# Kernel tuning notes

Measured on AMD Instinct MI355X. Metric: run time of the kernel, lower is better.

Reference implementation:

```python
import jax, jax.numpy as jnp
import numpy as np

SPATIAL_SHAPES = [(100, 152), (50, 76), (25, 38), (13, 19)]
D_MODEL = 256
N_HEADS = 8
N_LEVELS = 4
N_POINTS = 4
D_FFN = 1024
D_HEAD = D_MODEL // N_HEADS
EPS = 1e-5


def layernorm(x, g, b):
    mu = jnp.mean(x, axis=-1, keepdims=True)
    var = jnp.var(x, axis=-1, keepdims=True)
    return (x - mu) * jax.lax.rsqrt(var + EPS) * g + b


def bilinear_sample(value_l, H, W, locs):
    # value_l: (N, H*W, nH, dH); locs: (N, Lq, nH, P, 2) normalized to [0,1]
    # Matches torch grid_sample(align_corners=False, padding_mode='zeros') with grid=2*loc-1.
    N, Lq = locs.shape[0], locs.shape[1]
    x = locs[..., 0] * W - 0.5  # (N, Lq, nH, P) pixel coords
    y = locs[..., 1] * H - 0.5
    x0 = jnp.floor(x)
    y0 = jnp.floor(y)
    fx = x - x0
    fy = y - y0
    x0 = x0.astype(jnp.int32)
    y0 = y0.astype(jnp.int32)
    out = jnp.zeros((N, Lq, N_POINTS, N_HEADS, D_HEAD), value_l.dtype)
    for dy in (0, 1):
        for dx in (0, 1):
            xi = x0 + dx
            yi = y0 + dy
            w = (fx if dx else 1.0 - fx) * (fy if dy else 1.0 - fy)
            valid = (xi >= 0) & (xi < W) & (yi >= 0) & (yi < H)
            idx = jnp.clip(yi, 0, H - 1) * W + jnp.clip(xi, 0, W - 1)  # (N, Lq, nH, P)
            idx = idx.transpose(0, 1, 3, 2).reshape(N, Lq * N_POINTS, N_HEADS, 1)
            g = jnp.take_along_axis(value_l, idx, axis=1)  # (N, Lq*P, nH, dH)
            g = g.reshape(N, Lq, N_POINTS, N_HEADS, D_HEAD)
            wv = jnp.where(valid, w, 0.0).transpose(0, 1, 3, 2)[..., None]  # (N, Lq, P, nH, 1)
            out = out + g * wv
    return out  # (N, Lq, P, nH, dH)


def msdeform_attn(query, value_in, ref_points,
                  w_value, b_value, w_off, b_off, w_attn, b_attn, w_out, b_out):
    N, Lq, _ = query.shape
    value = (value_in @ w_value + b_value).reshape(N, -1, N_HEADS, D_HEAD)
    off = (query @ w_off + b_off).reshape(N, Lq, N_HEADS, N_LEVELS, N_POINTS, 2)
    attn = (query @ w_attn + b_attn).reshape(N, Lq, N_HEADS, N_LEVELS * N_POINTS)
    attn = jax.nn.softmax(attn, axis=-1).reshape(N, Lq, N_HEADS, N_LEVELS, N_POINTS)
    # offset normalizer is (W, H) per level
    norm = jnp.array([[w, h] for (h, w) in SPATIAL_SHAPES], dtype=query.dtype)  # (L, 2)
    locs = ref_points[:, :, None, :, None, :] + off / norm[None, None, None, :, None, :]
    out = jnp.zeros((N, Lq, N_HEADS, D_HEAD), query.dtype)
    start = 0
    for l, (H, W) in enumerate(SPATIAL_SHAPES):
        v_l = value[:, start:start + H * W]
        s = bilinear_sample(v_l, H, W, locs[:, :, :, l])  # (N, Lq, P, nH, dH)
        out = out + jnp.einsum('nqhp,nqphd->nqhd', attn[:, :, :, l], s)
        start += H * W
    out = out.reshape(N, Lq, D_MODEL)
    return out @ w_out + b_out


def setup_inputs() -> dict:
    key = jax.random.key(0)
    ks = jax.random.split(key, 20)
    B = 2
    Lq = sum(h * w for h, w in SPATIAL_SHAPES)  # 20197
    scale = 0.02
    inp = {
        'src': jax.random.normal(ks[0], (B, Lq, D_MODEL), jnp.float32),
        'pos': jax.random.normal(ks[1], (B, Lq, D_MODEL), jnp.float32),
        'reference_points': jax.random.uniform(ks[2], (B, Lq, N_LEVELS, 2), jnp.float32),
        'spatial_shapes': jnp.array(SPATIAL_SHAPES, dtype=jnp.int32),
        'level_start_index': jnp.array(np.cumsum([0] + [h * w for h, w in SPATIAL_SHAPES[:-1]]), dtype=jnp.int32),
        'w_value': jax.random.normal(ks[3], (D_MODEL, D_MODEL), jnp.float32) * scale,
        'b_value': jnp.zeros((D_MODEL,), jnp.float32),
        'w_off': jax.random.normal(ks[4], (D_MODEL, N_HEADS * N_LEVELS * N_POINTS * 2), jnp.float32) * scale,
        'b_off': jax.random.normal(ks[5], (N_HEADS * N_LEVELS * N_POINTS * 2,), jnp.float32) * scale,
        'w_attn': jax.random.normal(ks[6], (D_MODEL, N_HEADS * N_LEVELS * N_POINTS), jnp.float32) * scale,
        'b_attn': jnp.zeros((N_HEADS * N_LEVELS * N_POINTS,), jnp.float32),
        'w_out': jax.random.normal(ks[7], (D_MODEL, D_MODEL), jnp.float32) * scale,
        'b_out': jnp.zeros((D_MODEL,), jnp.float32),
        'g1': jnp.ones((D_MODEL,), jnp.float32),
        'beta1': jnp.zeros((D_MODEL,), jnp.float32),
        'w1': jax.random.normal(ks[8], (D_MODEL, D_FFN), jnp.float32) * scale,
        'b1': jnp.zeros((D_FFN,), jnp.float32),
        'w2': jax.random.normal(ks[9], (D_FFN, D_MODEL), jnp.float32) * scale,
        'b2': jnp.zeros((D_MODEL,), jnp.float32),
        'g2': jnp.ones((D_MODEL,), jnp.float32),
        'beta2': jnp.zeros((D_MODEL,), jnp.float32),
    }
    return inp


def reference(src, pos, reference_points, spatial_shapes, level_start_index,
              w_value, b_value, w_off, b_off, w_attn, b_attn, w_out, b_out,
              g1, beta1, w1, b1, w2, b2, g2, beta2):
    query = src + pos
    src2 = msdeform_attn(query, src, reference_points,
                         w_value, b_value, w_off, b_off, w_attn, b_attn, w_out, b_out)
    src = layernorm(src + src2, g1, beta1)
    h = jax.nn.relu(src @ w1 + b1)
    src = layernorm(src + h @ w2 + b2, g2, beta2)
    return src
```

## Files before the change

### kernel.cpp

```cpp
#include <hip/hip_runtime.h>

#define LQ   20197
#define MTOT 40394

typedef _Float16 f16;
typedef _Float16 f16x8 __attribute__((ext_vector_type(8)));
typedef _Float16 f16x4 __attribute__((ext_vector_type(4)));
typedef _Float16 f16x2 __attribute__((ext_vector_type(2)));
typedef float    f32x4 __attribute__((ext_vector_type(4)));

#define OFF_WT 0ull
#define OFF_B4 1507328ull
#define OFF_B1 42870784ull
#define OFF_B2 63552512ull
#define OFF_B3 84234240ull
#define OFF_B5 104915968ull
#define OFF_B6 125597696ull
#define OFF_B7 166961152ull

#define WT_V    0
#define WT_OFF  65536
#define WT_ATTN 131072
#define WT_OUT  163840
#define WT_W1   229376
#define WT_W2   491520
#define WT_TOTAL 753664
#define WCONV_TOTAL (WT_TOTAL + 384)

__device__ __forceinline__ void gload_lds16(const f16* g, f16* l) {
    __builtin_amdgcn_global_load_lds(
        (const __attribute__((address_space(1))) unsigned int*)g,
        (__attribute__((address_space(3))) unsigned int*)l,
        16, 0, 0);
}

__global__ __launch_bounds__(256) void k_wconv(
    const float* __restrict__ wv, const float* __restrict__ woff,
    const float* __restrict__ wattn, const float* __restrict__ wout,
    const float* __restrict__ w1, const float* __restrict__ w2,
    const float* __restrict__ boff, const float* __restrict__ battn,
    f16* __restrict__ dst, float* __restrict__ biasoa)
{
    int gid = blockIdx.x * 256 + threadIdx.x;
    if (gid >= WCONV_TOTAL) return;
    if (gid >= WT_TOTAL) {
        int i = gid - WT_TOTAL;
        biasoa[i] = (i < 256) ? boff[i] : battn[i - 256];
        return;
    }
    const float* src; int Kd, Nd, base;
    if      (gid < 65536)  { src = wv;    Kd = 256;  Nd = 256;  base = 0; }
    else if (gid < 131072) { src = woff;  Kd = 256;  Nd = 256;  base = 65536; }
    else if (gid < 163840) { src = wattn; Kd = 256;  Nd = 128;  base = 131072; }
    else if (gid < 229376) { src = wout;  Kd = 256;  Nd = 256;  base = 163840; }
    else if (gid < 491520) { src = w1;    Kd = 256;  Nd = 1024; base = 229376; }
    else                   { src = w2;    Kd = 1024; Nd = 256;  base = 491520; }
    int loc = gid - base;
    int n = loc % Nd, k = loc / Nd;
    dst[base + n * Kd + k] = (f16)src[k * Nd + n];
}

__global__ __launch_bounds__(256) void k_prep(
    const float* __restrict__ src, const float* __restrict__ pos,
    f16* __restrict__ srch, f16* __restrict__ qh, int total4)
{
    int i = blockIdx.x * 256 + threadIdx.x;
    if (i >= total4) return;
    float4 s = ((const float4*)src)[i];
    float4 p = ((const float4*)pos)[i];
    f16x4 hs = { (f16)s.x, (f16)s.y, (f16)s.z, (f16)s.w };
    f16x4 hq = { (f16)(s.x + p.x), (f16)(s.y + p.y), (f16)(s.z + p.z), (f16)(s.w + p.w) };
    ((f16x4*)srch)[i] = hs;
    ((f16x4*)qh)[i]   = hq;
}

template<bool RELU, int OUTM>
__global__ __launch_bounds__(256) void k_gemm128(
    const f16* __restrict__ A, const f16* __restrict__ Bt,
    const float* __restrict__ bias, void* __restrict__ Cout,
    int M, int N, int K)
{
    __shared__ __align__(16) char pool[34816];
    f16* const sm = (f16*)pool;

    const int NBn = N >> 7;
    const int MBn = (M + 127) >> 7;
    const int tiles = MBn * NBn;
    const int q = gridDim.x >> 3;
    const int bid = blockIdx.x;
    const int swz = (bid & 7) * q + (bid >> 3);
    if (swz >= tiles) return;
    const int m0 = (swz / NBn) << 7;
    const int n0 = (swz % NBn) << 7;

    const int t = threadIdx.x, wid = t >> 6, lane = t & 63;

    const int c0 = wid, c1 = wid + 4;
    const int sr = lane >> 2, sk = (lane & 3) * 8;
    const int ra0 = min(m0 + c0 * 16 + sr, M - 1);
    const int ra1 = min(m0 + c1 * 16 + sr, M - 1);
    const f16* pa0 = A + (size_t)ra0 * K + sk;
    const f16* pa1 = A + (size_t)ra1 * K + sk;
    const f16* pb0 = Bt + (size_t)(n0 + c0 * 16 + sr) * K + sk;
    const f16* pb1 = Bt + (size_t)(n0 + c1 * 16 + sr) * K + sk;
    const int lo0 = c0 * 512, lo1 = c1 * 512;

    const int wr = wid >> 1, wc = wid & 1;
    const int fr = lane & 15, kb = (lane >> 4) * 8;

    f32x4 acc[4][4] = {};
    const int NT = K >> 5;

    gload_lds16(pa0, sm + lo0);
    gload_lds16(pa1, sm + lo1);
    gload_lds16(pb0, sm + 4096 + lo0);
    gload_lds16(pb1, sm + 4096 + lo1);
    __syncthreads();

    for (int tt = 0; tt < NT; ++tt) {
        const int cur = (tt & 1) << 13, nxt = cur ^ 8192;
        if (tt + 1 < NT) {
            const int k0 = (tt + 1) << 5;
            gload_lds16(pa0 + k0, sm + nxt + lo0);
            gload_lds16(pa1 + k0, sm + nxt + lo1);
            gload_lds16(pb0 + k0, sm + nxt + 4096 + lo0);
            gload_lds16(pb1 + k0, sm + nxt + 4096 + lo1);
        }
        f16x8 af[4], bf[4];
#pragma unroll
        for (int i = 0; i < 4; ++i)
            af[i] = *(const f16x8*)&sm[cur + (wr * 64 + i * 16 + fr) * 32 + kb];
#pragma unroll
        for (int i = 0; i < 4; ++i)
            bf[i] = *(const f16x8*)&sm[cur + 4096 + (wc * 64 + i * 16 + fr) * 32 + kb];
#pragma unroll
        for (int mi = 0; mi < 4; ++mi)
#pragma unroll
            for (int ni = 0; ni < 4; ++ni)
                acc[mi][ni] = __builtin_amdgcn_mfma_f32_16x16x32_f16(af[mi], bf[ni], acc[mi][ni], 0, 0, 0);
        __syncthreads();
    }

    const int r4 = (lane >> 4) * 4;
#pragma unroll
    for (int ni = 0; ni < 4; ++ni) {
        const int lcol = wc * 64 + ni * 16 + fr;
        const float bv = bias[n0 + lcol];
#pragma unroll
        for (int mi = 0; mi < 4; ++mi) {
#pragma unroll
            for (int j = 0; j < 4; ++j) {
                float v = acc[mi][ni][j] + bv;
                if (RELU) v = fmaxf(v, 0.f);
                sm[(wr * 64 + mi * 16 + r4 + j) * 136 + lcol] = (f16)v;
            }
        }
    }
    __syncthreads();

    if (OUTM == 1) {
        const int rr = t >> 4, cc = (t & 15) * 8;
#pragma unroll
        for (int pass = 0; pass < 8; ++pass) {
            const int r = pass * 16 + rr;
            const int row = m0 + r;
            if (row < M) {
                f16x8 v = *(const f16x8*)&sm[r * 136 + cc];
                *(f16x8*)&((f16*)Cout)[(size_t)row * N + n0 + cc] = v;
            }
        }
    } else {
        const int cbl = t >> 6, rr = (t & 63) >> 2, cc = (t & 3) * 8;
        const size_t cb = (size_t)((n0 >> 5) + cbl);
#pragma unroll
        for (int pass = 0; pass < 8; ++pass) {
            const int r = pass * 16 + rr;
            const int row = m0 + r;
            if (row < M) {
                f16x8 v = *(const f16x8*)&sm[r * 136 + cbl * 32 + cc];
                *(f16x8*)&((f16*)Cout)[(cb * M + row) * 32 + cc] = v;
            }
        }
    }
}

__global__ __launch_bounds__(256) void k_sample(
    const f16* __restrict__ oa, const f16* __restrict__ valueT,
    const float* __restrict__ ref, f16* __restrict__ samp)
{
    __shared__ uint2 s_g[32][17];
    __shared__ f16x4 s_w[32][17];
    const int head = blockIdx.x & 7;
    const int tok0 = (blockIdx.x >> 3) * 32;
    const int t = threadIdx.x;

#pragma unroll
    for (int it = 0; it < 2; ++it) {
        const int tl = it * 16 + (t >> 4);
        const int lp = t & 15, l = lp >> 2;
        const int tok = tok0 + tl;
        if (tok < MTOT) {
            const size_t row = (size_t)tok * 384;
            float logit = (float)oa[row + 256 + head * 16 + lp];
            float mx = logit;
#pragma unroll
            for (int m = 1; m < 16; m <<= 1) mx = fmaxf(mx, __shfl_xor(mx, m));
            float e = __expf(logit - mx);
            float sum = e;
#pragma unroll
            for (int m = 1; m < 16; m <<= 1) sum += __shfl_xor(sum, m);
            const float aw = e / sum;

            const float fW = (l == 0) ? 152.f : (l == 1) ? 76.f : (l == 2) ? 38.f : 19.f;
            const float fH = (l == 0) ? 100.f : (l == 1) ? 50.f : (l == 2) ? 25.f : 13.f;
            const int   W  = (l == 0) ? 152 : (l == 1) ? 76 : (l == 2) ? 38 : 19;
            const int   H  = (l == 0) ? 100 : (l == 1) ? 50 : (l == 2) ? 25 : 13;
            const int   st = (l == 0) ? 0 : (l == 1) ? 15200 : (l == 2) ? 19000 : 19950;

            const f16x2 ov = *(const f16x2*)&oa[row + head * 32 + lp * 2];
            const float2 rxy = *(const float2*)&ref[(size_t)tok * 8 + l * 2];
            const float x = rxy.x * fW + (float)ov.x - 0.5f;
            const float y = rxy.y * fH + (float)ov.y - 0.5f;
            const float xf = floorf(x), yf = floorf(y);
            const float fx = x - xf, fy = y - yf;
            const int x0 = (int)xf, y0 = (int)yf;

            const bool vx0 = (x0 >= 0) && (x0 < W);
            const bool vx1 = (x0 >= -1) && (x0 < W - 1);
            const bool vy0 = (y0 >= 0) && (y0 < H);
            const bool vy1 = (y0 >= -1) && (y0 < H - 1);
            const int x0c = min(max(x0, 0), W - 1), x1c = min(max(x0 + 1, 0), W - 1);
            const int y0c = min(max(y0, 0), H - 1), y1c = min(max(y0 + 1, 0), H - 1);

            const int n = (tok >= LQ) ? 1 : 0;
            const unsigned int b00 = (unsigned int)(n * LQ + st + y0c * W + x0c) << 6;
            const unsigned int dx6 = (unsigned int)(x1c - x0c) << 6;
            const unsigned int dy6 = (unsigned int)((y1c - y0c) * W) << 6;
            s_g[tl][lp] = make_uint2(b00, dx6 | (dy6 << 16));

            const f16 w00 = (f16)((vx0 && vy0) ? (1.f - fx) * (1.f - fy) * aw : 0.f);
            const f16 w01 = (f16)((vx1 && vy0) ? fx * (1.f - fy) * aw : 0.f);
            const f16 w10 = (f16)((vx0 && vy1) ? (1.f - fx) * fy * aw : 0.f);
            const f16 w11 = (f16)((vx1 && vy1) ? fx * fy * aw : 0.f);
            f16x4 wv = { w00, w01, w10, w11 };
            s_w[tl][lp] = wv;
        }
    }
    __syncthreads();

    const int tl = t >> 3;
    const int sub = (t >> 2) & 1;
    const int l4 = t & 3;
    const int tok = tok0 + tl;
    if (tok >= MTOT) return;
    const unsigned int lb = (unsigned int)l4 * 16u;
    const char* vbase = (const char*)valueT + (size_t)head * (MTOT * 64ull);
    const int pbase = sub * 8;

    f16x2 a0 = {}, a1 = {}, a2 = {}, a3 = {};
#pragma unroll
    for (int pi = 0; pi < 8; ++pi) {
        const int p = pbase + pi;
        const uint2 g  = s_g[tl][p];
        const f16x4 wv = s_w[tl][p];
        const unsigned int a00 = g.x + lb;
        const unsigned int dx6 = g.y & 0xFFFFu;
        const unsigned int dy6 = g.y >> 16;
        const f16x8 v00 = *(const f16x8*)(vbase + a00);
        const f16x8 v01 = *(const f16x8*)(vbase + (a00 + dx6));
        const f16x8 v10 = *(const f16x8*)(vbase + (a00 + dy6));
        const f16x8 v11 = *(const f16x8*)(vbase + (a00 + dy6 + dx6));
        const f16x2 w0 = { wv[0], wv[0] }, w1 = { wv[1], wv[1] };
        const f16x2 w2 = { wv[2], wv[2] }, w3 = { wv[3], wv[3] };
        const f16x2* p0 = (const f16x2*)&v00;
        const f16x2* p1 = (const f16x2*)&v01;
        const f16x2* p2 = (const f16x2*)&v10;
        const f16x2* p3 = (const f16x2*)&v11;
        a0 = a0 + p0[0] * w0; a1 = a1 + p0[1] * w0;
        a2 = a2 + p0[2] * w0; a3 = a3 + p0[3] * w0;
        a0 = a0 + p1[0] * w1; a1 = a1 + p1[1] * w1;
        a2 = a2 + p1[2] * w1; a3 = a3 + p1[3] * w1;
        a0 = a0 + p2[0] * w2; a1 = a1 + p2[1] * w2;
        a2 = a2 + p2[2] * w2; a3 = a3 + p2[3] * w2;
        a0 = a0 + p3[0] * w3; a1 = a1 + p3[1] * w3;
        a2 = a2 + p3[2] * w3; a3 = a3 + p3[3] * w3;
    }

    union { f16x2 h; int i; } u0, u1, u2, u3;
    u0.h = a0; u1.h = a1; u2.h = a2; u3.h = a3;
    union { int i; f16x2 h; } r0, r1, r2, r3;
    r0.i = __shfl_xor(u0.i, 4); r1.i = __shfl_xor(u1.i, 4);
    r2.i = __shfl_xor(u2.i, 4); r3.i = __shfl_xor(u3.i, 4);
    a0 = a0 + r0.h; a1 = a1 + r1.h; a2 = a2 + r2.h; a3 = a3 + r3.h;

    f16x4 o = sub ? (f16x4){ a2.x, a2.y, a3.x, a3.y }
                  : (f16x4){ a0.x, a0.y, a1.x, a1.y };
    *(f16x4*)&samp[(size_t)tok * 256 + head * 32 + l4 * 8 + sub * 4] = o;
}

template<int OUTF16>
__global__ __launch_bounds__(256) void k_lnh(
    const f16* __restrict__ xa, const f16* __restrict__ xb,
    const float* __restrict__ g, const float* __restrict__ be,
    void* __restrict__ y, int M)
{
    const int row = blockIdx.x * 4 + (threadIdx.x >> 6);
    const int lane = threadIdx.x & 63;
    if (row >= M) return;
    const size_t o = (size_t)row * 256 + lane * 4;
    f16x4 a = *(const f16x4*)(xa + o);
    f16x4 b = *(const f16x4*)(xb + o);
    float x0 = (float)a.x + (float)b.x, x1 = (float)a.y + (float)b.y;
    float x2 = (float)a.z + (float)b.z, x3 = (float)a.w + (float)b.w;
    float s  = x0 + x1 + x2 + x3;
    float ss = x0*x0 + x1*x1 + x2*x2 + x3*x3;
#pragma unroll
    for (int m = 1; m < 64; m <<= 1) { s += __shfl_xor(s, m); ss += __shfl_xor(ss, m); }
    const float mean = s * (1.f / 256.f);
    const float var  = ss * (1.f / 256.f) - mean * mean;
    const float rstd = rsqrtf(var + 1e-5f);
    float4 gv = *(const float4*)(g + lane * 4);
    float4 bv = *(const float4*)(be + lane * 4);
    const float y0 = (x0 - mean) * rstd * gv.x + bv.x;
    const float y1 = (x1 - mean) * rstd * gv.y + bv.y;
    const float y2 = (x2 - mean) * rstd * gv.z + bv.z;
    const float y3 = (x3 - mean) * rstd * gv.w + bv.w;
    if (OUTF16) {
        f16x4 hv = { (f16)y0, (f16)y1, (f16)y2, (f16)y3 };
        *(f16x4*)((f16*)y + o) = hv;
    } else {
        float4 yo = { y0, y1, y2, y3 };
        *(float4*)((float*)y + o) = yo;
    }
}

extern "C" void kernel_launch(void* const* d_in, const int* in_sizes, int n_in,
                              void* d_out, int out_size, void* d_ws, size_t ws_size,
                              hipStream_t stream) {
    const float* src   = (const float*)d_in[0];
    const float* pos   = (const float*)d_in[1];
    const float* ref   = (const float*)d_in[2];
    const float* w_value = (const float*)d_in[5];
    const float* b_value = (const float*)d_in[6];
    const float* w_off   = (const float*)d_in[7];
    const float* b_off   = (const float*)d_in[8];
    const float* w_attn  = (const float*)d_in[9];
    const float* b_attn  = (const float*)d_in[10];
    const float* w_out   = (const float*)d_in[11];
    const float* b_out   = (const float*)d_in[12];
    const float* g1    = (const float*)d_in[13];
    const float* beta1 = (const float*)d_in[14];
    const float* w1    = (const float*)d_in[15];
    const float* b1    = (const float*)d_in[16];
    const float* w2    = (const float*)d_in[17];
    const float* b2    = (const float*)d_in[18];
    const float* g2    = (const float*)d_in[19];
    const float* beta2 = (const float*)d_in[20];

    char* ws = (char*)d_ws;
    f16*   wT      = (f16*)(ws + OFF_WT);
    f16*   oa      = (f16*)(ws + OFF_B4);
    f16*   y2h     = (f16*)(ws + OFF_B4);
    f16*   srch    = (f16*)(ws + OFF_B1);
    f16*   qh      = (f16*)(ws + OFF_B2);
    f16*   x1h     = (f16*)(ws + OFF_B2);
    f16*   valueT  = (f16*)(ws + OFF_B3);
    f16*   hh      = (f16*)(ws + OFF_B3);
    float* biasoa  = (float*)(ws + OFF_B5);
    f16*   src2h   = (f16*)(ws + OFF_B6);
    f16*   samph   = (f16*)(ws + OFF_B7);
    float* outp    = (float*)d_out;

    const int M = MTOT;
    const int MB = (M + 127) / 128;
    auto grid8 = [&](int nb) { return ((MB * nb) + 7) & ~7; };

    k_wconv<<<(WCONV_TOTAL + 255) / 256, 256, 0, stream>>>(
        w_value, w_off, w_attn, w_out, w1, w2, b_off, b_attn, wT, biasoa);
    k_prep<<<(M * 64 + 255) / 256, 256, 0, stream>>>(src, pos, srch, qh, M * 64);

    k_gemm128<false, 2><<<grid8(2), 256, 0, stream>>>(srch, wT + WT_V, b_value, valueT, M, 256, 256);
    k_gemm128<false, 1><<<grid8(3), 256, 0, stream>>>(qh, wT + WT_OFF, biasoa, oa, M, 384, 256);
    {
        const int nchunk = (MTOT + 31) / 32;
        k_sample<<<dim3(nchunk * 8), 256, 0, stream>>>(oa, valueT, ref, samph);
    }
    k_gemm128<false, 1><<<grid8(2), 256, 0, stream>>>(samph, wT + WT_OUT, b_out, src2h, M, 256, 256);
    k_lnh<1><<<(M + 3) / 4, 256, 0, stream>>>(srch, src2h, g1, beta1, x1h, M);
    k_gemm128<true, 1><<<grid8(8), 256, 0, stream>>>(x1h, wT + WT_W1, b1, hh, M, 1024, 256);
    k_gemm128<false, 1><<<grid8(2), 256, 0, stream>>>(hh, wT + WT_W2, b2, y2h, M, 256, 1024);
    k_lnh<0><<<(M + 3) / 4, 256, 0, stream>>>(x1h, y2h, g2, beta2, outp, M);

    (void)in_sizes; (void)n_in; (void)out_size; (void)ws_size;
}
```

Before: 223.7 us.

## Fuse residual add and LayerNorm into the N=256 output GEMMs

Adds a GEMM kernel that computes a 64-row by full-256-column tile, then adds bias and the residual and applies LayerNorm in the epilogue using a cross-wave reduction through shared memory. It replaces the output-projection GEMM plus LN1 and the FFN2 GEMM plus LN2, removing two intermediate f16 buffers and two separate LayerNorm launches. The cost is a 64-row tile that re-reads the full B matrix per block and keeps a large accumulator set in registers, which may lower occupancy and MFMA efficiency, especially for the K=1024 GEMM.

```diff
diff --git a/kernel.cpp b/kernel.cpp
--- a/kernel.cpp
+++ b/kernel.cpp
@@ -9,13 +9,11 @@
 typedef _Float16 f16x2 __attribute__((ext_vector_type(2)));
 typedef float    f32x4 __attribute__((ext_vector_type(4)));
 
-#define OFF_WT 0ull
 #define OFF_B4 1507328ull
 #define OFF_B1 42870784ull
 #define OFF_B2 63552512ull
 #define OFF_B3 84234240ull
 #define OFF_B5 104915968ull
-#define OFF_B6 125597696ull
 #define OFF_B7 166961152ull
 
 #define WT_V    0
@@ -179,6 +177,184 @@
             if (row < M) {
                 f16x8 v = *(const f16x8*)&sm[r * 136 + cbl * 32 + cc];
                 *(f16x8*)&((f16*)Cout)[(cb * M + row) * 32 + cc] = v;
+            }
+        }
+    }
+}
+
+template<int OUTF32>
+__global__ __launch_bounds__(256) void k_gemm_ln(
+    const f16* __restrict__ A, const f16* __restrict__ Bt,
+    const float* __restrict__ bias, const f16* __restrict__ resid,
+    const float* __restrict__ gw, const float* __restrict__ bw,
+    void* __restrict__ Out, int M, int K)
+{
+    __shared__ __align__(16) char pool[40960];
+    f16* const sm = (f16*)pool;
+
+    const int MBn = (M + 63) >> 6;
+    const int q = gridDim.x >> 3;
+    const int swz = ((int)blockIdx.x & 7) * q + ((int)blockIdx.x >> 3);
+    if (swz >= MBn) return;
+    const int m0 = swz << 6;
+
+    const int t = threadIdx.x, wid = t >> 6, lane = t & 63;
+    const int sr = lane >> 2, sk = (lane & 3) * 8;
+
+    const f16* gsrc[5];
+#pragma unroll
+    for (int i = 0; i < 5; ++i) {
+        const int c = wid + 4 * i;
+        const int row = c * 16 + sr;
+        if (row < 64) gsrc[i] = A + (size_t)min(m0 + row, M - 1) * K + sk;
+        else          gsrc[i] = Bt + (size_t)(row - 64) * K + sk;
+    }
+
+    const int fr = lane & 15, kb = (lane >> 4) * 8;
+    f32x4 acc[4][4] = {};
+    const int NT = K >> 5;
+
+#pragma unroll
+    for (int i = 0; i < 5; ++i)
+        gload_lds16(gsrc[i], sm + (wid + 4 * i) * 512);
+    __syncthreads();
+
+    for (int tt = 0; tt < NT; ++tt) {
+        const int cur = (tt & 1) * 10240, nxt = cur ^ 10240;
+        if (tt + 1 < NT) {
+            const int k0 = (tt + 1) << 5;
+#pragma unroll
+            for (int i = 0; i < 5; ++i)
+                gload_lds16(gsrc[i] + k0, sm + nxt + (wid + 4 * i) * 512);
+        }
+        f16x8 af[4], bf[4];
+#pragma unroll
+        for (int i = 0; i < 4; ++i)
+            af[i] = *(const f16x8*)&sm[cur + (i * 16 + fr) * 32 + kb];
+#pragma unroll
+        for (int i = 0; i < 4; ++i)
+            bf[i] = *(const f16x8*)&sm[cur + 2048 + (wid * 64 + i * 16 + fr) * 32 + kb];
+#pragma unroll
+        for (int mi = 0; mi < 4; ++mi)
+#pragma unroll
+            for (int ni = 0; ni < 4; ++ni)
+                acc[mi][ni] = __builtin_amdgcn_mfma_f32_16x16x32_f16(af[mi], bf[ni], acc[mi][ni], 0, 0, 0);
+        __syncthreads();
+    }
+
+#pragma unroll
+    for (int i = 0; i < 8; ++i) {
+        const int row = i * 8 + (t >> 5);
+        const int col = (t & 31) * 8;
+        const int gr = min(m0 + row, M - 1);
+        *(f16x8*)&sm[row * 264 + col] = *(const f16x8*)&resid[(size_t)gr * 256 + col];
+    }
+    __syncthreads();
+
+    const int r4 = (lane >> 4) * 4;
+    const int colb = wid * 64;
+    float bv[4], gv[4], bev[4];
+#pragma unroll
+    for (int ni = 0; ni < 4; ++ni) {
+        bv[ni]  = bias[colb + ni * 16 + fr];
+        gv[ni]  = gw[colb + ni * 16 + fr];
+        bev[ni] = bw[colb + ni * 16 + fr];
+    }
+    float s[4][4] = {}, ssq[4][4] = {};
+#pragma unroll
+    for (int mi = 0; mi < 4; ++mi)
+#pragma unroll
+        for (int j = 0; j < 4; ++j) {
+            const int rl = mi * 16 + r4 + j;
+#pragma unroll
+            for (int ni = 0; ni < 4; ++ni) {
+                float v = acc[mi][ni][j] + bv[ni] + (float)sm[rl * 264 + colb + ni * 16 + fr];
+                acc[mi][ni][j] = v;
+                s[mi][j] += v; ssq[mi][j] += v * v;
+            }
+        }
+#pragma unroll
+    for (int mi = 0; mi < 4; ++mi)
+#pragma unroll
+        for (int j = 0; j < 4; ++j)
+#pragma unroll
+            for (int m = 1; m < 16; m <<= 1) {
+                s[mi][j]   += __shfl_xor(s[mi][j], m);
+                ssq[mi][j] += __shfl_xor(ssq[mi][j], m);
+            }
+    float2* R = (float2*)(pool + 33792);
+    if (fr == 0) {
+#pragma unroll
+        for (int mi = 0; mi < 4; ++mi)
+#pragma unroll
+            for (int j = 0; j < 4; ++j) {
+                float2 v2 = { s[mi][j], ssq[mi][j] };
+                R[(mi * 16 + r4 + j) * 4 + wid] = v2;
+            }
+    }
+    __syncthreads();
+    float2* Mr = (float2*)(pool + 35840);
+    if (t < 64) {
+        float s4 = 0.f, q4 = 0.f;
+#pragma unroll
+        for (int w = 0; w < 4; ++w) { float2 rv = R[t * 4 + w]; s4 += rv.x; q4 += rv.y; }
+        const float mean = s4 * (1.f / 256.f);
+        const float var  = q4 * (1.f / 256.f) - mean * mean;
+        float2 mv = { mean, rsqrtf(var + 1e-5f) };
+        Mr[t] = mv;
+    }
+    __syncthreads();
+
+    if (OUTF32 == 0) {
+        f16* Out16 = (f16*)Out;
+#pragma unroll
+        for (int mi = 0; mi < 4; ++mi)
+#pragma unroll
+            for (int j = 0; j < 4; ++j) {
+                const int rl = mi * 16 + r4 + j;
+                const float2 mr = Mr[rl];
+#pragma unroll
+                for (int ni = 0; ni < 4; ++ni) {
+                    const float y = (acc[mi][ni][j] - mr.x) * mr.y * gv[ni] + bev[ni];
+                    sm[rl * 264 + colb + ni * 16 + fr] = (f16)y;
+                }
+            }
+        __syncthreads();
+#pragma unroll
+        for (int i = 0; i < 8; ++i) {
+            const int row = i * 8 + (t >> 5);
+            const int col = (t & 31) * 8;
+            if (m0 + row < M)
+                *(f16x8*)&Out16[(size_t)(m0 + row) * 256 + col] = *(const f16x8*)&sm[row * 264 + col];
+        }
+    } else {
+        float* OutF = (float*)Out;
+        float* Y = (float*)pool;
+#pragma unroll
+        for (int pass = 0; pass < 2; ++pass) {
+            __syncthreads();
+            if ((wid >> 1) == pass) {
+                const int cb2 = (wid & 1) * 64;
+#pragma unroll
+                for (int mi = 0; mi < 4; ++mi)
+#pragma unroll
+                    for (int j = 0; j < 4; ++j) {
+                        const int rl = mi * 16 + r4 + j;
+                        const float2 mr = Mr[rl];
+#pragma unroll
+                        for (int ni = 0; ni < 4; ++ni)
+                            Y[rl * 132 + cb2 + ni * 16 + fr] =
+                                (acc[mi][ni][j] - mr.x) * mr.y * gv[ni] + bev[ni];
+                    }
+            }
+            __syncthreads();
+#pragma unroll
+            for (int i = 0; i < 8; ++i) {
+                const int row = i * 8 + (t >> 5);
+                const int col = (t & 31) * 4;
+                if (m0 + row < M)
+                    *(float4*)&OutF[(size_t)(m0 + row) * 256 + pass * 128 + col] =
+                        *(const float4*)&Y[row * 132 + col];
             }
         }
     }
@@ -298,42 +474,6 @@
     *(f16x4*)&samp[(size_t)tok * 256 + head * 32 + l4 * 8 + sub * 4] = o;
 }
 
-template<int OUTF16>
-__global__ __launch_bounds__(256) void k_lnh(
-    const f16* __restrict__ xa, const f16* __restrict__ xb,
-    const float* __restrict__ g, const float* __restrict__ be,
-    void* __restrict__ y, int M)
-{
-    const int row = blockIdx.x * 4 + (threadIdx.x >> 6);
-    const int lane = threadIdx.x & 63;
-    if (row >= M) return;
-    const size_t o = (size_t)row * 256 + lane * 4;
-    f16x4 a = *(const f16x4*)(xa + o);
-    f16x4 b = *(const f16x4*)(xb + o);
-    float x0 = (float)a.x + (float)b.x, x1 = (float)a.y + (float)b.y;
-    float x2 = (float)a.z + (float)b.z, x3 = (float)a.w + (float)b.w;
-    float s  = x0 + x1 + x2 + x3;
-    float ss = x0*x0 + x1*x1 + x2*x2 + x3*x3;
-#pragma unroll
-    for (int m = 1; m < 64; m <<= 1) { s += __shfl_xor(s, m); ss += __shfl_xor(ss, m); }
-    const float mean = s * (1.f / 256.f);
-    const float var  = ss * (1.f / 256.f) - mean * mean;
-    const float rstd = rsqrtf(var + 1e-5f);
-    float4 gv = *(const float4*)(g + lane * 4);
-    float4 bv = *(const float4*)(be + lane * 4);
-    const float y0 = (x0 - mean) * rstd * gv.x + bv.x;
-    const float y1 = (x1 - mean) * rstd * gv.y + bv.y;
-    const float y2 = (x2 - mean) * rstd * gv.z + bv.z;
-    const float y3 = (x3 - mean) * rstd * gv.w + bv.w;
-    if (OUTF16) {
-        f16x4 hv = { (f16)y0, (f16)y1, (f16)y2, (f16)y3 };
-        *(f16x4*)((f16*)y + o) = hv;
-    } else {
-        float4 yo = { y0, y1, y2, y3 };
-        *(float4*)((float*)y + o) = yo;
-    }
-}
-
 extern "C" void kernel_launch(void* const* d_in, const int* in_sizes, int n_in,
                               void* d_out, int out_size, void* d_ws, size_t ws_size,
                               hipStream_t stream) {
@@ -358,22 +498,22 @@
     const float* beta2 = (const float*)d_in[20];
 
     char* ws = (char*)d_ws;
-    f16*   wT      = (f16*)(ws + OFF_WT);
+    f16*   wT      = (f16*)(ws + 0);
     f16*   oa      = (f16*)(ws + OFF_B4);
-    f16*   y2h     = (f16*)(ws + OFF_B4);
     f16*   srch    = (f16*)(ws + OFF_B1);
     f16*   qh      = (f16*)(ws + OFF_B2);
     f16*   x1h     = (f16*)(ws + OFF_B2);
     f16*   valueT  = (f16*)(ws + OFF_B3);
     f16*   hh      = (f16*)(ws + OFF_B3);
     float* biasoa  = (float*)(ws + OFF_B5);
-    f16*   src2h   = (f16*)(ws + OFF_B6);
     f16*   samph   = (f16*)(ws + OFF_B7);
     float* outp    = (float*)d_out;
 
     const int M = MTOT;
     const int MB = (M + 127) / 128;
     auto grid8 = [&](int nb) { return ((MB * nb) + 7) & ~7; };
+    const int MB64 = (M + 63) / 64;
+    const int grid64 = (MB64 + 7) & ~7;
 
     k_wconv<<<(WCONV_TOTAL + 255) / 256, 256, 0, stream>>>(
         w_value, w_off, w_attn, w_out, w1, w2, b_off, b_attn, wT, biasoa);
@@ -385,11 +525,9 @@
         const int nchunk = (MTOT + 31) / 32;
         k_sample<<<dim3(nchunk * 8), 256, 0, stream>>>(oa, valueT, ref, samph);
     }
-    k_gemm128<false, 1><<<grid8(2), 256, 0, stream>>>(samph, wT + WT_OUT, b_out, src2h, M, 256, 256);
-    k_lnh<1><<<(M + 3) / 4, 256, 0, stream>>>(srch, src2h, g1, beta1, x1h, M);
+    k_gemm_ln<0><<<grid64, 256, 0, stream>>>(samph, wT + WT_OUT, b_out, srch, g1, beta1, x1h, M, 256);
     k_gemm128<true, 1><<<grid8(8), 256, 0, stream>>>(x1h, wT + WT_W1, b1, hh, M, 1024, 256);
-    k_gemm128<false, 1><<<grid8(2), 256, 0, stream>>>(hh, wT + WT_W2, b2, y2h, M, 256, 1024);
-    k_lnh<0><<<(M + 3) / 4, 256, 0, stream>>>(x1h, y2h, g2, beta2, outp, M);
+    k_gemm_ln<1><<<grid64, 256, 0, stream>>>(hh, wT + WT_W2, b2, x1h, g2, beta2, outp, M, 1024);
 
     (void)in_sizes; (void)n_in; (void)out_size; (void)ws_size;
 }
```

After: 236.3 us. +5.6%, slower.

## Fuse FFN up and down projections into one kernel keeping hidden in LDS

Applied to the files above, without the earlier changes.

Replaces the two separate FFN GEMM launches with a single kernel that processes 32-row tiles. It computes relu(x1·W1+b1) into a swizzled LDS buffer, then multiplies that buffer by W2 directly. This removes the global write and re-read of the 1024-wide hidden activation. In exchange it uses 80KB of LDS per block, which limits occupancy, and it reads weight B fragments straight from global/L2 with no LDS staging. Each block also reloads the full W1 and W2.

```diff
diff --git a/kernel.cpp b/kernel.cpp
--- a/kernel.cpp
+++ b/kernel.cpp
@@ -9,7 +9,6 @@
 typedef _Float16 f16x2 __attribute__((ext_vector_type(2)));
 typedef float    f32x4 __attribute__((ext_vector_type(4)));
 
-#define OFF_WT 0ull
 #define OFF_B4 1507328ull
 #define OFF_B1 42870784ull
 #define OFF_B2 63552512ull
@@ -180,6 +179,112 @@
                 f16x8 v = *(const f16x8*)&sm[r * 136 + cbl * 32 + cc];
                 *(f16x8*)&((f16*)Cout)[(cb * M + row) * 32 + cc] = v;
             }
+        }
+    }
+}
+
+__global__ __launch_bounds__(256) void k_ffn(
+    const f16* __restrict__ x1, const f16* __restrict__ w1t,
+    const float* __restrict__ b1, const f16* __restrict__ w2t,
+    const float* __restrict__ b2, f16* __restrict__ y2, int M)
+{
+    __shared__ __align__(16) char pool[81920];
+    f16* const A_lds = (f16*)pool;
+    f16* const h_lds = (f16*)pool + 8192;
+    f16* const epi   = (f16*)pool;
+
+    const int nblk = (M + 31) >> 5;
+    const int q = gridDim.x >> 3;
+    const int swz = ((int)blockIdx.x & 7) * q + ((int)blockIdx.x >> 3);
+    if (swz >= nblk) return;
+    const int m0 = swz << 5;
+
+    const int t = threadIdx.x, w = t >> 6, lane = t & 63;
+    const int fr = lane & 15, qd = lane >> 4;
+    const int kb = qd * 8, r4 = qd * 4;
+
+#pragma unroll
+    for (int i = 0; i < 4; ++i) {
+        const int id = w * 4 + i, c = id >> 1, half = id & 1;
+        const int row = min(m0 + half * 16 + (lane >> 2), M - 1);
+        gload_lds16(x1 + (size_t)row * 256 + c * 32 + (lane & 3) * 8,
+                    A_lds + c * 1024 + half * 512);
+    }
+    __syncthreads();
+
+    for (int nc = 0; nc < 8; ++nc) {
+        f32x4 acc1[2][2] = {};
+        const int nbase = nc * 128 + w * 32;
+#pragma unroll 2
+        for (int kc = 0; kc < 8; ++kc) {
+            f16x8 af[2], bf[2];
+#pragma unroll
+            for (int mi = 0; mi < 2; ++mi)
+                af[mi] = *(const f16x8*)&A_lds[kc * 1024 + (mi * 16 + fr) * 32 + kb];
+#pragma unroll
+            for (int ni = 0; ni < 2; ++ni)
+                bf[ni] = *(const f16x8*)&w1t[(size_t)(nbase + ni * 16 + fr) * 256 + kc * 32 + kb];
+#pragma unroll
+            for (int mi = 0; mi < 2; ++mi)
+#pragma unroll
+                for (int ni = 0; ni < 2; ++ni)
+                    acc1[mi][ni] = __builtin_amdgcn_mfma_f32_16x16x32_f16(af[mi], bf[ni], acc1[mi][ni], 0, 0, 0);
+        }
+        const int hc = nc * 4 + w;
+#pragma unroll
+        for (int ni = 0; ni < 2; ++ni) {
+            const float bv = b1[nbase + ni * 16 + fr];
+            const int col = ni * 16 + fr;
+#pragma unroll
+            for (int mi = 0; mi < 2; ++mi)
+#pragma unroll
+                for (int j = 0; j < 4; ++j) {
+                    const int row = mi * 16 + r4 + j;
+                    const float v = fmaxf(acc1[mi][ni][j] + bv, 0.f);
+                    const int g = (col >> 3) ^ ((row >> 2) & 3);
+                    h_lds[hc * 1024 + row * 32 + g * 8 + (col & 7)] = (f16)v;
+                }
+        }
+    }
+    __syncthreads();
+
+    f32x4 acc2[2][4] = {};
+    const int swzg = (qd ^ ((fr >> 2) & 3)) << 3;
+#pragma unroll 2
+    for (int kc = 0; kc < 32; ++kc) {
+        f16x8 af[2], bf[4];
+#pragma unroll
+        for (int mi = 0; mi < 2; ++mi)
+            af[mi] = *(const f16x8*)&h_lds[kc * 1024 + (mi * 16 + fr) * 32 + swzg];
+#pragma unroll
+        for (int ni = 0; ni < 4; ++ni)
+            bf[ni] = *(const f16x8*)&w2t[(size_t)(w * 64 + ni * 16 + fr) * 1024 + kc * 32 + kb];
+#pragma unroll
+        for (int mi = 0; mi < 2; ++mi)
+#pragma unroll
+            for (int ni = 0; ni < 4; ++ni)
+                acc2[mi][ni] = __builtin_amdgcn_mfma_f32_16x16x32_f16(af[mi], bf[ni], acc2[mi][ni], 0, 0, 0);
+    }
+    __syncthreads();
+
+#pragma unroll
+    for (int ni = 0; ni < 4; ++ni) {
+        const int col = w * 64 + ni * 16 + fr;
+        const float bv = b2[col];
+#pragma unroll
+        for (int mi = 0; mi < 2; ++mi)
+#pragma unroll
+            for (int j = 0; j < 4; ++j)
+                epi[(mi * 16 + r4 + j) * 264 + col] = (f16)(acc2[mi][ni][j] + bv);
+    }
+    __syncthreads();
+    {
+        const int row = t >> 3, cb = (t & 7) * 32;
+        if (m0 + row < M) {
+#pragma unroll
+            for (int i = 0; i < 4; ++i)
+                *(f16x8*)&y2[(size_t)(m0 + row) * 256 + cb + i * 8] =
+                    *(const f16x8*)&epi[row * 264 + cb + i * 8];
         }
     }
 }
@@ -358,14 +463,13 @@
     const float* beta2 = (const float*)d_in[20];
 
     char* ws = (char*)d_ws;
-    f16*   wT      = (f16*)(ws + OFF_WT);
+    f16*   wT      = (f16*)(ws + 0);
     f16*   oa      = (f16*)(ws + OFF_B4);
     f16*   y2h     = (f16*)(ws + OFF_B4);
     f16*   srch    = (f16*)(ws + OFF_B1);
     f16*   qh      = (f16*)(ws + OFF_B2);
     f16*   x1h     = (f16*)(ws + OFF_B2);
     f16*   valueT  = (f16*)(ws + OFF_B3);
-    f16*   hh      = (f16*)(ws + OFF_B3);
     float* biasoa  = (float*)(ws + OFF_B5);
     f16*   src2h   = (f16*)(ws + OFF_B6);
     f16*   samph   = (f16*)(ws + OFF_B7);
@@ -387,8 +491,11 @@
     }
     k_gemm128<false, 1><<<grid8(2), 256, 0, stream>>>(samph, wT + WT_OUT, b_out, src2h, M, 256, 256);
     k_lnh<1><<<(M + 3) / 4, 256, 0, stream>>>(srch, src2h, g1, beta1, x1h, M);
-    k_gemm128<true, 1><<<grid8(8), 256, 0, stream>>>(x1h, wT + WT_W1, b1, hh, M, 1024, 256);
-    k_gemm128<false, 1><<<grid8(2), 256, 0, stream>>>(hh, wT + WT_W2, b2, y2h, M, 256, 1024);
+    {
+        const int nblk = (M + 31) / 32;
+        const int g = (nblk + 7) & ~7;
+        k_ffn<<<dim3(g), 256, 0, stream>>>(x1h, wT + WT_W1, b1, wT + WT_W2, b2, y2h, M);
+    }
     k_lnh<0><<<(M + 3) / 4, 256, 0, stream>>>(x1h, y2h, g2, beta2, outp, M);
 
     (void)in_sizes; (void)n_in; (void)out_size; (void)ws_size;
```

Result: slower. 340.2 us (+52.1%).

## Fuse weight conversion with input prep and give each sampling thread all points

Applied to the files above, without the earlier changes.

Merges the weight transpose/convert kernel and the src/pos fp16 prep kernel into one launch, removing a kernel launch and its tail. The sampling kernel now processes 64 tokens per block, and each thread accumulates all 16 sampling points for its 8-channel slice. This removes the cross-lane shuffle reduction and writes 16-byte outputs. In exchange, each thread runs a longer serial loop of gathers, so fewer independent threads are available to hide memory latency.

```diff
diff --git a/kernel.cpp b/kernel.cpp
--- a/kernel.cpp
+++ b/kernel.cpp
@@ -9,7 +9,6 @@
 typedef _Float16 f16x2 __attribute__((ext_vector_type(2)));
 typedef float    f32x4 __attribute__((ext_vector_type(4)));
 
-#define OFF_WT 0ull
 #define OFF_B4 1507328ull
 #define OFF_B1 42870784ull
 #define OFF_B2 63552512ull
@@ -26,6 +25,8 @@
 #define WT_W2   491520
 #define WT_TOTAL 753664
 #define WCONV_TOTAL (WT_TOTAL + 384)
+#define PREP_TOTAL (MTOT * 64)
+#define FUSED_TOTAL (WCONV_TOTAL + PREP_TOTAL)
 
 __device__ __forceinline__ void gload_lds16(const f16* g, f16* l) {
     __builtin_amdgcn_global_load_lds(
@@ -34,15 +35,27 @@
         16, 0, 0);
 }
 
-__global__ __launch_bounds__(256) void k_wconv(
+__global__ __launch_bounds__(256) void k_wconv_prep(
     const float* __restrict__ wv, const float* __restrict__ woff,
     const float* __restrict__ wattn, const float* __restrict__ wout,
     const float* __restrict__ w1, const float* __restrict__ w2,
     const float* __restrict__ boff, const float* __restrict__ battn,
-    f16* __restrict__ dst, float* __restrict__ biasoa)
+    f16* __restrict__ dst, float* __restrict__ biasoa,
+    const float* __restrict__ srcf, const float* __restrict__ posf,
+    f16* __restrict__ srch, f16* __restrict__ qh)
 {
     int gid = blockIdx.x * 256 + threadIdx.x;
-    if (gid >= WCONV_TOTAL) return;
+    if (gid >= FUSED_TOTAL) return;
+    if (gid >= WCONV_TOTAL) {
+        const int i = gid - WCONV_TOTAL;
+        float4 s = ((const float4*)srcf)[i];
+        float4 p = ((const float4*)posf)[i];
+        f16x4 hs = { (f16)s.x, (f16)s.y, (f16)s.z, (f16)s.w };
+        f16x4 hq = { (f16)(s.x + p.x), (f16)(s.y + p.y), (f16)(s.z + p.z), (f16)(s.w + p.w) };
+        ((f16x4*)srch)[i] = hs;
+        ((f16x4*)qh)[i]   = hq;
+        return;
+    }
     if (gid >= WT_TOTAL) {
         int i = gid - WT_TOTAL;
         biasoa[i] = (i < 256) ? boff[i] : battn[i - 256];
@@ -60,20 +73,6 @@
     dst[base + n * Kd + k] = (f16)src[k * Nd + n];
 }
 
-__global__ __launch_bounds__(256) void k_prep(
-    const float* __restrict__ src, const float* __restrict__ pos,
-    f16* __restrict__ srch, f16* __restrict__ qh, int total4)
-{
-    int i = blockIdx.x * 256 + threadIdx.x;
-    if (i >= total4) return;
-    float4 s = ((const float4*)src)[i];
-    float4 p = ((const float4*)pos)[i];
-    f16x4 hs = { (f16)s.x, (f16)s.y, (f16)s.z, (f16)s.w };
-    f16x4 hq = { (f16)(s.x + p.x), (f16)(s.y + p.y), (f16)(s.z + p.z), (f16)(s.w + p.w) };
-    ((f16x4*)srch)[i] = hs;
-    ((f16x4*)qh)[i]   = hq;
-}
-
 template<bool RELU, int OUTM>
 __global__ __launch_bounds__(256) void k_gemm128(
     const f16* __restrict__ A, const f16* __restrict__ Bt,
@@ -188,14 +187,14 @@
     const f16* __restrict__ oa, const f16* __restrict__ valueT,
     const float* __restrict__ ref, f16* __restrict__ samp)
 {
-    __shared__ uint2 s_g[32][17];
-    __shared__ f16x4 s_w[32][17];
+    __shared__ uint2 s_g[64][17];
+    __shared__ f16x4 s_w[64][17];
     const int head = blockIdx.x & 7;
-    const int tok0 = (blockIdx.x >> 3) * 32;
+    const int tok0 = (blockIdx.x >> 3) * 64;
     const int t = threadIdx.x;
 
 #pragma unroll
-    for (int it = 0; it < 2; ++it) {
+    for (int it = 0; it < 4; ++it) {
         const int tl = it * 16 + (t >> 4);
         const int lp = t & 15, l = lp >> 2;
         const int tok = tok0 + tl;
@@ -248,19 +247,15 @@
     }
     __syncthreads();
 
-    const int tl = t >> 3;
-    const int sub = (t >> 2) & 1;
-    const int l4 = t & 3;
+    const int tl = t >> 2, l4 = t & 3;
     const int tok = tok0 + tl;
     if (tok >= MTOT) return;
     const unsigned int lb = (unsigned int)l4 * 16u;
     const char* vbase = (const char*)valueT + (size_t)head * (MTOT * 64ull);
-    const int pbase = sub * 8;
 
     f16x2 a0 = {}, a1 = {}, a2 = {}, a3 = {};
-#pragma unroll
-    for (int pi = 0; pi < 8; ++pi) {
-        const int p = pbase + pi;
+#pragma unroll 4
+    for (int p = 0; p < 16; ++p) {
         const uint2 g  = s_g[tl][p];
         const f16x4 wv = s_w[tl][p];
         const unsigned int a00 = g.x + lb;
@@ -285,17 +280,8 @@
         a0 = a0 + p3[0] * w3; a1 = a1 + p3[1] * w3;
         a2 = a2 + p3[2] * w3; a3 = a3 + p3[3] * w3;
     }
-
-    union { f16x2 h; int i; } u0, u1, u2, u3;
-    u0.h = a0; u1.h = a1; u2.h = a2; u3.h = a3;
-    union { int i; f16x2 h; } r0, r1, r2, r3;
-    r0.i = __shfl_xor(u0.i, 4); r1.i = __shfl_xor(u1.i, 4);
-    r2.i = __shfl_xor(u2.i, 4); r3.i = __shfl_xor(u3.i, 4);
-    a0 = a0 + r0.h; a1 = a1 + r1.h; a2 = a2 + r2.h; a3 = a3 + r3.h;
-
-    f16x4 o = sub ? (f16x4){ a2.x, a2.y, a3.x, a3.y }
-                  : (f16x4){ a0.x, a0.y, a1.x, a1.y };
-    *(f16x4*)&samp[(size_t)tok * 256 + head * 32 + l4 * 8 + sub * 4] = o;
+    f16x8 o = { a0.x, a0.y, a1.x, a1.y, a2.x, a2.y, a3.x, a3.y };
+    *(f16x8*)&samp[(size_t)tok * 256 + head * 32 + l4 * 8] = o;
 }
 
 template<int OUTF16>
@@ -358,7 +344,7 @@
     const float* beta2 = (const float*)d_in[20];
 
     char* ws = (char*)d_ws;
-    f16*   wT      = (f16*)(ws + OFF_WT);
+    f16*   wT      = (f16*)(ws + 0);
     f16*   oa      = (f16*)(ws + OFF_B4);
     f16*   y2h     = (f16*)(ws + OFF_B4);
     f16*   srch    = (f16*)(ws + OFF_B1);
@@ -375,14 +361,14 @@
     const int MB = (M + 127) / 128;
     auto grid8 = [&](int nb) { return ((MB * nb) + 7) & ~7; };
 
-    k_wconv<<<(WCONV_TOTAL + 255) / 256, 256, 0, stream>>>(
-        w_value, w_off, w_attn, w_out, w1, w2, b_off, b_attn, wT, biasoa);
-    k_prep<<<(M * 64 + 255) / 256, 256, 0, stream>>>(src, pos, srch, qh, M * 64);
+    k_wconv_prep<<<(FUSED_TOTAL + 255) / 256, 256, 0, stream>>>(
+        w_value, w_off, w_attn, w_out, w1, w2, b_off, b_attn, wT, biasoa,
+        src, pos, srch, qh);
 
     k_gemm128<false, 2><<<grid8(2), 256, 0, stream>>>(srch, wT + WT_V, b_value, valueT, M, 256, 256);
     k_gemm128<false, 1><<<grid8(3), 256, 0, stream>>>(qh, wT + WT_OFF, biasoa, oa, M, 384, 256);
     {
-        const int nchunk = (MTOT + 31) / 32;
+        const int nchunk = (MTOT + 63) / 64;
         k_sample<<<dim3(nchunk * 8), 256, 0, stream>>>(oa, valueT, ref, samph);
     }
     k_gemm128<false, 1><<<grid8(2), 256, 0, stream>>>(samph, wT + WT_OUT, b_out, src2h, M, 256, 256);
```

Result: no change. 220.4 us (-1.4%).
